# Performance work log

Hardware: AMD Instinct MI355X
Metric: run time of the kernel (lower is better)

Reference implementation:

```python
import jax, jax.numpy as jnp
import numpy as np

N, K, H = 98, 10, 4        # landmarks, neighbors/node, heads
B, CIN, HC = 1024, 256, 64 # batch, in_channels, head_channels
NEG = -9e15


def setup_inputs() -> dict:
    key = jax.random.key(0)
    ks = jax.random.split(key, 3)
    rng = np.random.default_rng(0)
    # fixed sparsity pattern: K unique neighbors per row, row-major order
    cols2d = np.stack([np.sort(rng.choice(N, K, replace=False)) for _ in range(N)])
    rows = np.repeat(np.arange(N), K)
    cols = cols2d.reshape(-1)
    x = jax.random.normal(ks[0], (B, N, CIN), jnp.float32)
    W = jax.random.normal(ks[1], (H, 2, CIN, HC), jnp.float32) * 0.05  # xavier-ish
    e = jnp.ones((H, N * K), jnp.float32)  # nn.init.constant_(e, 1)
    stdv = 1.0 / np.sqrt(HC)
    bias = jax.random.uniform(ks[2], (H, HC), jnp.float32, -stdv, stdv)
    return {"x": x, "W": W, "e": e, "bias": bias,
            "rows": jnp.asarray(rows, jnp.int32),
            "cols": jnp.asarray(cols, jnp.int32)}


def reference(x, W, e, bias, rows, cols):
    # h0/h1 for all heads at once: [2, H, B, N, HC]
    h = jnp.einsum('bnc,hscd->shbnd', x, W)
    h0, h1 = h[0], h[1]
    # masked adjacency logits per head: -9e15 everywhere, learned e at edges
    base = jnp.full((N, N), NEG, jnp.float32)
    logits = jax.vmap(lambda eh: base.at[rows, cols].set(eh))(e)  # [H,N,N]
    A = jax.nn.softmax(logits, axis=-1)  # F.softmax(adj, dim=1) on [N,N]
    diag = jnp.diagonal(A, axis1=-2, axis2=-1)  # [H,N] -> adj*M part
    A_off = A - diag[..., None] * jnp.eye(N, dtype=A.dtype)  # adj*(1-M)
    out = diag[:, None, :, None] * h0 + jnp.einsum('hij,hbjd->hbid', A_off, h1)
    out = out + bias[:, None, None, :]  # [H,B,N,HC]
    # concat heads along channel dim -> [B, N, H*HC]
    return jnp.transpose(out, (1, 2, 0, 3)).reshape(B, N, H * HC)
```

## Files before the change

### kernel.cpp

```cpp
#include <hip/hip_runtime.h>

typedef __bf16 bf16;
typedef bf16 bf16x4 __attribute__((ext_vector_type(4)));
typedef bf16 bf16x8 __attribute__((ext_vector_type(8)));
typedef _Float16 half_t;
typedef half_t half4 __attribute__((ext_vector_type(4)));
typedef half_t half8 __attribute__((ext_vector_type(8)));
typedef float f32x4 __attribute__((ext_vector_type(4)));

#define NND 98
#define KNB 10
#define NH 4
#define CIN 256
#define HC 64
#define KAG 224
#define SROW 232
#define XA_TILE (7 * 8 * 64 * 8)

#define WP_OFF   0
#define WP_BYTES 262144
#define G2D_OFF  (WP_OFF + WP_BYTES)
#define G2D_BYTES (NH * 112 * KAG * 2)
#define G2A_OFF  (G2D_OFF + G2D_BYTES)
#define G2A_BYTES (NH * 49 * 64 * 8 * 2)
#define XA_OFF   (G2A_OFF + G2A_BYTES)

__device__ __forceinline__ bf16x8 load_a8(const float* p) {
  f32x4 u = *(const f32x4*)p;
  f32x4 v = *(const f32x4*)(p + 4);
  bf16x8 a;
  a[0] = (bf16)u[0]; a[1] = (bf16)u[1]; a[2] = (bf16)u[2]; a[3] = (bf16)u[3];
  a[4] = (bf16)v[0]; a[5] = (bf16)v[1]; a[6] = (bf16)v[2]; a[7] = (bf16)v[3];
  return a;
}

__global__ __launch_bounds__(256) void misc1_kernel(const float* __restrict__ W,
                                                    bf16* __restrict__ Wp,
                                                    const float* __restrict__ e,
                                                    const int* __restrict__ cols,
                                                    half_t* __restrict__ G2d) {
  if (blockIdx.x < 64) {
    int t = blockIdx.x * 256 + threadIdx.x;
    int lane = t & 63;
    int nt = (t >> 6) & 3;
    int kt = (t >> 8) & 7;
    int hs = t >> 11;
    int n = nt * 16 + (lane & 15);
    int kb = kt * 32 + (lane >> 4) * 8;
    const float* src = W + (hs * CIN + kb) * HC + n;
    bf16x8 v;
#pragma unroll
    for (int j = 0; j < 8; ++j) v[j] = (bf16)src[j * HC];
    *(bf16x8*)(Wp + (long long)t * 8) = v;
    return;
  }
  const int h = blockIdx.x - 64;
  half_t* g = G2d + h * 112 * KAG;
  for (int i = threadIdx.x; i < 112 * KAG / 2; i += 256) ((unsigned int*)g)[i] = 0u;
  __syncthreads();
  const int i = threadIdx.x;
  if (i < NND) {
    const int* cp = cols + i * KNB;
    const float* ep = e + (h * NND + i) * KNB;
    float ev[KNB];
    int cv[KNB];
    float mx = -3.0e38f;
#pragma unroll
    for (int j = 0; j < KNB; ++j) { cv[j] = cp[j]; ev[j] = ep[j]; mx = fmaxf(mx, ev[j]); }
    float s = 0.f;
#pragma unroll
    for (int j = 0; j < KNB; ++j) { ev[j] = __expf(ev[j] - mx); s += ev[j]; }
    const float inv = 1.f / s;
    float dg = 0.f;
#pragma unroll
    for (int j = 0; j < KNB; ++j) {
      float wj = ev[j] * inv;
      if (cv[j] == i) { dg = wj; wj = 0.f; }
      g[i * KAG + cv[j]] = (half_t)wj;
    }
    g[i * KAG + 112 + i] = (half_t)dg;
  }
}

__global__ __launch_bounds__(256) void misc2_kernel(const half_t* __restrict__ G2d,
                                                    half_t* __restrict__ G2a,
                                                    const float* __restrict__ x,
                                                    bf16* __restrict__ xa, int B) {
  if (blockIdx.x < 49) {
    int t = blockIdx.x * 256 + threadIdx.x;
    int lane = t & 63;
    int q = t >> 6;
    int kt = q % 7;
    int mt = (q / 7) % 7;
    int h = q / 49;
    int row = mt * 16 + (lane & 15);
    int k0 = kt * 32 + (lane >> 4) * 8;
    half8 v = *(const half8*)(G2d + (h * 112 + row) * KAG + k0);
    *(half8*)(G2a + (long long)t * 8) = v;
    return;
  }
  const int Bq = (B + 3) >> 2;
  int u = (blockIdx.x - 49) * 256 + threadIdx.x;
  if (u >= Bq * 7 * 8 * 64) return;
  const int lane = u & 63;
  const int kt = (u >> 6) & 7;
  const int v = u >> 9;
  const int b0 = v / 7;
  const int mt = v - b0 * 7;
  const int row = mt * 16 + (lane & 15);
  const int k0 = kt * 32 + (lane >> 4) * 8;
  bf16x8 a[4];
#pragma unroll
  for (int q = 0; q < 4; ++q) {
    const int b = b0 + Bq * q;
    a[q] = bf16x8{};
    if (b < B && row < NND) a[q] = load_a8(x + ((long long)b * NND + row) * CIN + k0);
  }
#pragma unroll
  for (int q = 0; q < 4; ++q) {
    const int b = b0 + Bq * q;
    if (b < B)
      *(bf16x8*)(xa + ((((long long)b * 7 + mt) * 8 + kt) * 64 + lane) * 8) = a[q];
  }
}

__global__ __launch_bounds__(512, 4) void semgconv_kernel(
    const bf16* __restrict__ xa, const half_t* __restrict__ G2a,
    const bf16* __restrict__ Wp, const float* __restrict__ bias,
    float* __restrict__ out, int nwg) {
  __shared__ __align__(16) unsigned char smem[65536];
  bf16* Wl = (bf16*)smem;
  half_t* S = (half_t*)smem;

  const int tid = threadIdx.x;
  const int lane = tid & 63;
  const int wv = tid >> 6;

  int n = blockIdx.x;
  int w = ((nwg & 7) == 0) ? ((n & 7) * (nwg >> 3) + (n >> 3)) : n;
  const int bp = w >> 2;
  const int h = w & 3;
  const int b0 = bp * 2;

  {
    const f32x4* src = (const f32x4*)(Wp + (long long)h * 32768);
    f32x4* dst = (f32x4*)smem;
#pragma unroll
    for (int it = 0; it < 8; ++it) {
      const int idx = tid + it * 512;
      dst[idx] = src[idx];
    }
  }
  __syncthreads();

  const int wm = wv & 3;
  const int sh = wv >> 2;
  const int mt0 = wm * 2;
  const bool has1 = (mt0 + 1 < 7);

  f32x4 acc[2][2][4] = {};
  {
    const bf16* wll = Wl + sh * 16384 + lane * 8;
    const bf16* ax0 = xa + (((long long)b0 * 7 + mt0) * 8 * 64 + lane) * 8;
    const bf16* ax1 = ax0 + XA_TILE;
#pragma unroll
    for (int kt = 0; kt < 8; ++kt) {
      bf16x8 a00 = *(const bf16x8*)(ax0 + kt * 512);
      bf16x8 a10 = *(const bf16x8*)(ax1 + kt * 512);
      bf16x8 a01 = {}, a11 = {};
      if (has1) {
        a01 = *(const bf16x8*)(ax0 + 4096 + kt * 512);
        a11 = *(const bf16x8*)(ax1 + 4096 + kt * 512);
      }
      bf16x8 bfr[4];
#pragma unroll
      for (int nt = 0; nt < 4; ++nt)
        bfr[nt] = *(const bf16x8*)(wll + (kt * 4 + nt) * 512);
#pragma unroll
      for (int nt = 0; nt < 4; ++nt) {
        acc[0][0][nt] = __builtin_amdgcn_mfma_f32_16x16x32_bf16(a00, bfr[nt], acc[0][0][nt], 0, 0, 0);
        acc[1][0][nt] = __builtin_amdgcn_mfma_f32_16x16x32_bf16(a10, bfr[nt], acc[1][0][nt], 0, 0, 0);
      }
      if (has1) {
#pragma unroll
        for (int nt = 0; nt < 4; ++nt) {
          acc[0][1][nt] = __builtin_amdgcn_mfma_f32_16x16x32_bf16(a01, bfr[nt], acc[0][1][nt], 0, 0, 0);
          acc[1][1][nt] = __builtin_amdgcn_mfma_f32_16x16x32_bf16(a11, bfr[nt], acc[1][1][nt], 0, 0, 0);
        }
      }
    }
  }
  __syncthreads();

  {
    const int jb = (sh ? 0 : 112) + (lane >> 4) * 4;
    const int cb = lane & 15;
#pragma unroll
    for (int it2 = 0; it2 < 2; ++it2) {
#pragma unroll
      for (int im = 0; im < 2; ++im) {
        if (mt0 + im < 7) {
          const int j0 = jb + (mt0 + im) * 16;
#pragma unroll
          for (int nt = 0; nt < 4; ++nt) {
            half4 hv;
            hv[0] = (half_t)acc[it2][im][nt][0];
            hv[1] = (half_t)acc[it2][im][nt][1];
            hv[2] = (half_t)acc[it2][im][nt][2];
            hv[3] = (half_t)acc[it2][im][nt][3];
            *(half4*)(&S[it2 * (64 * SROW) + (nt * 16 + cb) * SROW + j0]) = hv;
          }
        }
      }
    }
  }
  __syncthreads();

  const int it2 = wv & 1;
  const int wm2 = wv >> 1;
  const int mt0b = wm2 * 2;
  const bool has1b = (mt0b + 1 < 7);
  f32x4 a2[2][4] = {};
  {
    const half_t* g2l = G2a + ((long long)(h * 49 + mt0b * 7) * 64 + lane) * 8;
    const half_t* sl = S + it2 * (64 * SROW) + (lane & 15) * SROW + (lane >> 4) * 8;
#pragma unroll
    for (int kt = 0; kt < 7; ++kt) {
      half8 bfr[4];
#pragma unroll
      for (int nt = 0; nt < 4; ++nt)
        bfr[nt] = *(const half8*)(sl + nt * 16 * SROW + kt * 32);
      half8 af0 = *(const half8*)(g2l + (long long)kt * 512);
      half8 af1 = {};
      if (has1b) af1 = *(const half8*)(g2l + (long long)(7 + kt) * 512);
#pragma unroll
      for (int nt = 0; nt < 4; ++nt) {
        a2[0][nt] = __builtin_amdgcn_mfma_f32_16x16x32_f16(af0, bfr[nt], a2[0][nt], 0, 0, 0);
        if (has1b)
          a2[1][nt] = __builtin_amdgcn_mfma_f32_16x16x32_f16(af1, bfr[nt], a2[1][nt], 0, 0, 0);
      }
    }
  }

  {
    const int cb = lane & 15;
    const int r0 = (lane >> 4) * 4;
    float bs[4];
#pragma unroll
    for (int nt = 0; nt < 4; ++nt) bs[nt] = bias[h * HC + nt * 16 + cb];
    float* ob = out + (long long)(b0 + it2) * NND * (NH * HC) + h * HC + cb;
#pragma unroll
    for (int im = 0; im < 2; ++im) {
      const int mt = mt0b + im;
      if (mt < 7) {
#pragma unroll
        for (int r = 0; r < 4; ++r) {
          const int row = mt * 16 + r0 + r;
          if (row < NND) {
#pragma unroll
            for (int nt = 0; nt < 4; ++nt)
              ob[(long long)row * (NH * HC) + nt * 16] = a2[im][nt][r] + bs[nt];
          }
        }
      }
    }
  }
}

extern "C" void kernel_launch(void* const* d_in, const int* in_sizes, int n_in,
                              void* d_out, int out_size, void* d_ws, size_t ws_size,
                              hipStream_t stream) {
  const float* x    = (const float*)d_in[0];
  const float* W    = (const float*)d_in[1];
  const float* e    = (const float*)d_in[2];
  const float* bias = (const float*)d_in[3];
  const int* cols   = (const int*)d_in[5];
  float* out        = (float*)d_out;

  int B = in_sizes[0] / (NND * CIN);

  bf16* Wp    = (bf16*)((char*)d_ws + WP_OFF);
  half_t* G2d = (half_t*)((char*)d_ws + G2D_OFF);
  half_t* G2a = (half_t*)((char*)d_ws + G2A_OFF);
  bf16* xa    = (bf16*)((char*)d_ws + XA_OFF);

  misc1_kernel<<<68, 256, 0, stream>>>(W, Wp, e, cols, G2d);
  const int Bq = (B + 3) >> 2;
  const int xa_blocks = (Bq * 7 * 8 * 64 + 255) / 256;
  misc2_kernel<<<49 + xa_blocks, 256, 0, stream>>>(G2d, G2a, x, xa, B);

  const int nwg = (B / 2) * NH;
  semgconv_kernel<<<nwg, 512, 0, stream>>>(xa, G2a, Wp, bias, out, nwg);
}
```

Baseline: 243.8 us.

## Merge prep kernels via shared-memory adjacency build and prefetch MFMA operands

```diff
diff --git a/kernel.cpp b/kernel.cpp
--- a/kernel.cpp
+++ b/kernel.cpp
@@ -19,9 +19,7 @@
 
 #define WP_OFF   0
 #define WP_BYTES 262144
-#define G2D_OFF  (WP_OFF + WP_BYTES)
-#define G2D_BYTES (NH * 112 * KAG * 2)
-#define G2A_OFF  (G2D_OFF + G2D_BYTES)
+#define G2A_OFF  (WP_OFF + WP_BYTES)
 #define G2A_BYTES (NH * 49 * 64 * 8 * 2)
 #define XA_OFF   (G2A_OFF + G2A_BYTES)
 
@@ -34,11 +32,13 @@
   return a;
 }
 
-__global__ __launch_bounds__(256) void misc1_kernel(const float* __restrict__ W,
-                                                    bf16* __restrict__ Wp,
-                                                    const float* __restrict__ e,
-                                                    const int* __restrict__ cols,
-                                                    half_t* __restrict__ G2d) {
+__global__ __launch_bounds__(256) void prep_kernel(const float* __restrict__ W,
+                                                   bf16* __restrict__ Wp,
+                                                   const float* __restrict__ e,
+                                                   const int* __restrict__ cols,
+                                                   half_t* __restrict__ G2a,
+                                                   const float* __restrict__ x,
+                                                   bf16* __restrict__ xa, int B) {
   if (blockIdx.x < 64) {
     int t = blockIdx.x * 256 + threadIdx.x;
     int lane = t & 63;
@@ -54,53 +54,49 @@
     *(bf16x8*)(Wp + (long long)t * 8) = v;
     return;
   }
-  const int h = blockIdx.x - 64;
-  half_t* g = G2d + h * 112 * KAG;
-  for (int i = threadIdx.x; i < 112 * KAG / 2; i += 256) ((unsigned int*)g)[i] = 0u;
-  __syncthreads();
-  const int i = threadIdx.x;
-  if (i < NND) {
-    const int* cp = cols + i * KNB;
-    const float* ep = e + (h * NND + i) * KNB;
-    float ev[KNB];
-    int cv[KNB];
-    float mx = -3.0e38f;
-#pragma unroll
-    for (int j = 0; j < KNB; ++j) { cv[j] = cp[j]; ev[j] = ep[j]; mx = fmaxf(mx, ev[j]); }
-    float s = 0.f;
-#pragma unroll
-    for (int j = 0; j < KNB; ++j) { ev[j] = __expf(ev[j] - mx); s += ev[j]; }
-    const float inv = 1.f / s;
-    float dg = 0.f;
-#pragma unroll
-    for (int j = 0; j < KNB; ++j) {
-      float wj = ev[j] * inv;
-      if (cv[j] == i) { dg = wj; wj = 0.f; }
-      g[i * KAG + cv[j]] = (half_t)wj;
-    }
-    g[i * KAG + 112 + i] = (half_t)dg;
-  }
-}
-
-__global__ __launch_bounds__(256) void misc2_kernel(const half_t* __restrict__ G2d,
-                                                    half_t* __restrict__ G2a,
-                                                    const float* __restrict__ x,
-                                                    bf16* __restrict__ xa, int B) {
-  if (blockIdx.x < 49) {
-    int t = blockIdx.x * 256 + threadIdx.x;
-    int lane = t & 63;
-    int q = t >> 6;
-    int kt = q % 7;
-    int mt = (q / 7) % 7;
-    int h = q / 49;
-    int row = mt * 16 + (lane & 15);
-    int k0 = kt * 32 + (lane >> 4) * 8;
-    half8 v = *(const half8*)(G2d + (h * 112 + row) * KAG + k0);
-    *(half8*)(G2a + (long long)t * 8) = v;
+  if (blockIdx.x < 68) {
+    __shared__ __align__(16) half_t g[112 * KAG];
+    const int h = blockIdx.x - 64;
+    const int tid = threadIdx.x;
+    for (int i = tid; i < 112 * KAG / 2; i += 256) ((unsigned int*)g)[i] = 0u;
+    __syncthreads();
+    if (tid < NND) {
+      const int i = tid;
+      const int* cp = cols + i * KNB;
+      const float* ep = e + (h * NND + i) * KNB;
+      float ev[KNB];
+      int cv[KNB];
+      float mx = -3.0e38f;
+#pragma unroll
+      for (int j = 0; j < KNB; ++j) { cv[j] = cp[j]; ev[j] = ep[j]; mx = fmaxf(mx, ev[j]); }
+      float s = 0.f;
+#pragma unroll
+      for (int j = 0; j < KNB; ++j) { ev[j] = __expf(ev[j] - mx); s += ev[j]; }
+      const float inv = 1.f / s;
+      float dg = 0.f;
+#pragma unroll
+      for (int j = 0; j < KNB; ++j) {
+        float wj = ev[j] * inv;
+        if (cv[j] == i) { dg = wj; wj = 0.f; }
+        g[i * KAG + cv[j]] = (half_t)wj;
+      }
+      g[i * KAG + 112 + i] = (half_t)dg;
+    }
+    __syncthreads();
+    for (int u = tid; u < 49 * 64; u += 256) {
+      const int lane = u & 63;
+      const int q = u >> 6;
+      const int kt = q % 7;
+      const int mt = q / 7;
+      const int row = mt * 16 + (lane & 15);
+      const int k0 = kt * 32 + (lane >> 4) * 8;
+      half8 v = *(const half8*)(g + row * KAG + k0);
+      *(half8*)(G2a + (((long long)h * 49 + q) * 64 + lane) * 8) = v;
+    }
     return;
   }
   const int Bq = (B + 3) >> 2;
-  int u = (blockIdx.x - 49) * 256 + threadIdx.x;
+  int u = (blockIdx.x - 68) * 256 + threadIdx.x;
   if (u >= Bq * 7 * 8 * 64) return;
   const int lane = u & 63;
   const int kt = (u >> 6) & 7;
@@ -142,35 +138,45 @@
   const int h = w & 3;
   const int b0 = bp * 2;
 
-  {
-    const f32x4* src = (const f32x4*)(Wp + (long long)h * 32768);
-    f32x4* dst = (f32x4*)smem;
-#pragma unroll
-    for (int it = 0; it < 8; ++it) {
-      const int idx = tid + it * 512;
-      dst[idx] = src[idx];
-    }
-  }
-  __syncthreads();
-
   const int wm = wv & 3;
   const int sh = wv >> 2;
   const int mt0 = wm * 2;
   const bool has1 = (mt0 + 1 < 7);
 
+  const bf16* ax0 = xa + (((long long)b0 * 7 + mt0) * 8 * 64 + lane) * 8;
+  const bf16* ax1 = ax0 + XA_TILE;
+  bf16x8 a00 = *(const bf16x8*)(ax0);
+  bf16x8 a10 = *(const bf16x8*)(ax1);
+  bf16x8 a01 = {}, a11 = {};
+  if (has1) {
+    a01 = *(const bf16x8*)(ax0 + 4096);
+    a11 = *(const bf16x8*)(ax1 + 4096);
+  }
+
+  {
+    const f32x4* src = (const f32x4*)(Wp + (long long)h * 32768);
+    f32x4* dst = (f32x4*)smem;
+#pragma unroll
+    for (int it = 0; it < 8; ++it) {
+      const int idx = tid + it * 512;
+      dst[idx] = src[idx];
+    }
+  }
+  __syncthreads();
+
   f32x4 acc[2][2][4] = {};
   {
     const bf16* wll = Wl + sh * 16384 + lane * 8;
-    const bf16* ax0 = xa + (((long long)b0 * 7 + mt0) * 8 * 64 + lane) * 8;
-    const bf16* ax1 = ax0 + XA_TILE;
 #pragma unroll
     for (int kt = 0; kt < 8; ++kt) {
-      bf16x8 a00 = *(const bf16x8*)(ax0 + kt * 512);
-      bf16x8 a10 = *(const bf16x8*)(ax1 + kt * 512);
-      bf16x8 a01 = {}, a11 = {};
-      if (has1) {
-        a01 = *(const bf16x8*)(ax0 + 4096 + kt * 512);
-        a11 = *(const bf16x8*)(ax1 + 4096 + kt * 512);
+      bf16x8 n00, n10, n01, n11;
+      if (kt < 7) {
+        n00 = *(const bf16x8*)(ax0 + (kt + 1) * 512);
+        n10 = *(const bf16x8*)(ax1 + (kt + 1) * 512);
+        if (has1) {
+          n01 = *(const bf16x8*)(ax0 + 4096 + (kt + 1) * 512);
+          n11 = *(const bf16x8*)(ax1 + 4096 + (kt + 1) * 512);
+        }
       }
       bf16x8 bfr[4];
 #pragma unroll
@@ -188,6 +194,7 @@
           acc[1][1][nt] = __builtin_amdgcn_mfma_f32_16x16x32_bf16(a11, bfr[nt], acc[1][1][nt], 0, 0, 0);
         }
       }
+      a00 = n00; a10 = n10; a01 = n01; a11 = n11;
     }
   }
   __syncthreads();
@@ -224,21 +231,27 @@
   {
     const half_t* g2l = G2a + ((long long)(h * 49 + mt0b * 7) * 64 + lane) * 8;
     const half_t* sl = S + it2 * (64 * SROW) + (lane & 15) * SROW + (lane >> 4) * 8;
+    half8 af0 = *(const half8*)(g2l);
+    half8 af1 = {};
+    if (has1b) af1 = *(const half8*)(g2l + 7 * 512);
 #pragma unroll
     for (int kt = 0; kt < 7; ++kt) {
+      half8 n0, n1;
+      if (kt < 6) {
+        n0 = *(const half8*)(g2l + (long long)(kt + 1) * 512);
+        if (has1b) n1 = *(const half8*)(g2l + (long long)(8 + kt) * 512);
+      }
       half8 bfr[4];
 #pragma unroll
       for (int nt = 0; nt < 4; ++nt)
         bfr[nt] = *(const half8*)(sl + nt * 16 * SROW + kt * 32);
-      half8 af0 = *(const half8*)(g2l + (long long)kt * 512);
-      half8 af1 = {};
-      if (has1b) af1 = *(const half8*)(g2l + (long long)(7 + kt) * 512);
 #pragma unroll
       for (int nt = 0; nt < 4; ++nt) {
         a2[0][nt] = __builtin_amdgcn_mfma_f32_16x16x32_f16(af0, bfr[nt], a2[0][nt], 0, 0, 0);
         if (has1b)
           a2[1][nt] = __builtin_amdgcn_mfma_f32_16x16x32_f16(af1, bfr[nt], a2[1][nt], 0, 0, 0);
       }
+      af0 = n0; af1 = n1;
     }
   }
 
@@ -280,14 +293,12 @@
   int B = in_sizes[0] / (NND * CIN);
 
   bf16* Wp    = (bf16*)((char*)d_ws + WP_OFF);
-  half_t* G2d = (half_t*)((char*)d_ws + G2D_OFF);
   half_t* G2a = (half_t*)((char*)d_ws + G2A_OFF);
   bf16* xa    = (bf16*)((char*)d_ws + XA_OFF);
 
-  misc1_kernel<<<68, 256, 0, stream>>>(W, Wp, e, cols, G2d);
   const int Bq = (B + 3) >> 2;
   const int xa_blocks = (Bq * 7 * 8 * 64 + 255) / 256;
-  misc2_kernel<<<49 + xa_blocks, 256, 0, stream>>>(G2d, G2a, x, xa, B);
+  prep_kernel<<<68 + xa_blocks, 256, 0, stream>>>(W, Wp, e, cols, G2a, x, xa, B);
 
   const int nwg = (B / 2) * NH;
   semgconv_kernel<<<nwg, 512, 0, stream>>>(xa, G2a, Wp, bias, out, nwg);
```

New measurement: 230.5 us. -5.5%, faster.
